# Kernel optimization log

Measured on AMD Instinct MI355X. Metric: run time of the kernel, lower is better.

The kernel has to match this reference:

```python
import jax, jax.numpy as jnp
import numpy as np

N_NODES = 102400
N_EDGES = 1638400
DIMS = [128, 64, 32, 1]  # decoder_dim=128, decoder_l=3, last layer -> 1


def setup_inputs() -> dict:
    key = jax.random.key(0)
    ks = jax.random.split(key, 10)
    inp = {
        'b_z': jax.random.normal(ks[0], (N_NODES, DIMS[0]), jnp.float32),
        'src': jax.random.randint(ks[1], (N_EDGES,), 0, N_NODES, jnp.int64 if jax.config.jax_enable_x64 else jnp.int32),
        'dst': jax.random.randint(ks[2], (N_EDGES,), 0, N_NODES, jnp.int64 if jax.config.jax_enable_x64 else jnp.int32),
        'edge_weight': jax.random.uniform(ks[3], (N_EDGES,), jnp.float32),
        'b_size': 100,
    }
    # GraphConv weights: W [in, out], bias [out] (DGL xavier init; randn ok for ref)
    for i in range(3):
        inp[f'W{i}'] = jax.random.normal(ks[4 + i], (DIMS[i], DIMS[i + 1]), jnp.float32) * (1.0 / np.sqrt(DIMS[i]))
        inp[f'b{i}'] = jnp.zeros((DIMS[i + 1],), jnp.float32)
    return inp


def _gcn_layer(h, src, dst, ew, W, b, activate):
    n = h.shape[0]
    ones = jnp.ones((src.shape[0],), h.dtype)
    # norm='both': symmetric degree normalization with plain (unweighted) degrees
    out_deg = jnp.clip(jax.ops.segment_sum(ones, src, num_segments=n), 1.0)
    in_deg = jnp.clip(jax.ops.segment_sum(ones, dst, num_segments=n), 1.0)
    h = h * (out_deg ** -0.5)[:, None]
    h = h @ W  # in_feats > out_feats: transform before aggregation (DGL order)
    msg = h[src] * ew[:, None]           # [E, out] edge-weighted gather
    agg = jax.ops.segment_sum(msg, dst, num_segments=n)  # scatter-add
    agg = agg * (in_deg ** -0.5)[:, None] + b
    return jnp.tanh(agg) if activate else agg


def reference(b_z, src, dst, edge_weight, b_size, W0, b0, W1, b1, W2, b2):
    h = b_z
    h = _gcn_layer(h, src, dst, edge_weight, W0, b0, True)
    h = _gcn_layer(h, src, dst, edge_weight, W1, b1, True)
    h = _gcn_layer(h, src, dst, edge_weight, W2, b2, False)
    return h.reshape(b_size, -1)
```

## Files before the change

kernel.cpp:

```cpp
#include <hip/hip_runtime.h>
#include <hip/hip_fp16.h>
#include <math.h>

#define N_NODES 102400
#define N_EDGES 1638400
#define NB 100
#define PB 256
#define EPB (N_EDGES/PB)

union H4 { int2 i2; __half h[4]; };

typedef _Float16 f16;
typedef __attribute__((ext_vector_type(8))) _Float16 f16x8;
typedef __attribute__((ext_vector_type(4))) float f32x4;

__global__ __launch_bounds__(256) void fusedA_kernel(
    const int* __restrict__ src, const int* __restrict__ dst,
    int* __restrict__ histD, int* __restrict__ histS,
    const float* __restrict__ h, const float* __restrict__ W, __half* __restrict__ out) {
    const int tid = threadIdx.x;

    if (blockIdx.x < PB) {
        __shared__ int hD[NB], hS[NB];
        if (tid < NB) { hD[tid] = 0; hS[tid] = 0; }
        __syncthreads();
        int base = blockIdx.x * EPB;
        for (int i = tid; i < EPB; i += 256) {
            atomicAdd(&hD[dst[base + i] >> 10], 1);
            atomicAdd(&hS[src[base + i] >> 10], 1);
        }
        __syncthreads();
        if (tid < NB) {
            histD[blockIdx.x * NB + tid] = hD[tid];
            histS[blockIdx.x * NB + tid] = hS[tid];
        }
        return;
    }

    const int lane = tid & 63;
    const int wid = tid >> 6;
    const int lr = lane & 15;
    const int kg = lane >> 4;
    const long bbase = (long)(blockIdx.x - PB) * 256 + wid * 16;

    f16x8 bf[4][4];
    #pragma unroll
    for (int ks = 0; ks < 4; ++ks)
        #pragma unroll
        for (int ct = 0; ct < 4; ++ct)
            #pragma unroll
            for (int j = 0; j < 8; ++j)
                bf[ks][ct][j] = (f16)W[(ks * 32 + kg * 8 + j) * 64 + ct * 16 + lr];

    #pragma unroll
    for (int t = 0; t < 4; ++t) {
        const long rowbase = bbase + t * 64;
        const float* hrow = h + (rowbase + lr) * 128 + kg * 8;
        f32x4 acc[4] = {{0,0,0,0},{0,0,0,0},{0,0,0,0},{0,0,0,0}};
        #pragma unroll
        for (int ks = 0; ks < 4; ++ks) {
            const float4 a0 = *(const float4*)(hrow + ks * 32);
            const float4 a1 = *(const float4*)(hrow + ks * 32 + 4);
            f16x8 af;
            af[0] = (f16)a0.x; af[1] = (f16)a0.y; af[2] = (f16)a0.z; af[3] = (f16)a0.w;
            af[4] = (f16)a1.x; af[5] = (f16)a1.y; af[6] = (f16)a1.z; af[7] = (f16)a1.w;
            #pragma unroll
            for (int ct = 0; ct < 4; ++ct)
                acc[ct] = __builtin_amdgcn_mfma_f32_16x16x32_f16(af, bf[ks][ct], acc[ct], 0, 0, 0);
        }
        #pragma unroll
        for (int ct = 0; ct < 4; ++ct)
            #pragma unroll
            for (int r = 0; r < 4; ++r)
                out[(rowbase + kg * 4 + r) * 64 + ct * 16 + lr] = __float2half_rn(acc[ct][r]);
    }
}

__global__ __launch_bounds__(256) void scanB_kernel(const int* __restrict__ histD, const int* __restrict__ histS,
                                                    int* __restrict__ offD, int* __restrict__ offS,
                                                    int* __restrict__ coarseD, int* __restrict__ coarseS) {
    __shared__ int totD[NB], totS[NB], baseD[NB + 1], baseS[NB + 1];
    int t = threadIdx.x;
    if (t < NB) { int s = 0; for (int k = 0; k < PB; k++) s += histD[k * NB + t]; totD[t] = s; }
    else if (t >= 128 && t < 128 + NB) { int j = t - 128; int s = 0; for (int k = 0; k < PB; k++) s += histS[k * NB + j]; totS[j] = s; }
    __syncthreads();
    if (t == 0)   { int r = 0; for (int j = 0; j < NB; j++) { baseD[j] = r; r += totD[j]; } baseD[NB] = r; }
    if (t == 128) { int r = 0; for (int j = 0; j < NB; j++) { baseS[j] = r; r += totS[j]; } baseS[NB] = r; }
    __syncthreads();
    if (t < NB) { int r = baseD[t]; for (int k = 0; k < PB; k++) { offD[k * NB + t] = r; r += histD[k * NB + t]; } }
    else if (t >= 128 && t < 128 + NB) { int j = t - 128; int r = baseS[j]; for (int k = 0; k < PB; k++) { offS[k * NB + j] = r; r += histS[k * NB + j]; } }
    if (t <= NB) coarseD[t] = baseD[t];
    if (t >= 128 && t <= 128 + NB) coarseS[t - 128] = baseS[t - 128];
}

__global__ __launch_bounds__(256) void partC_kernel(const int* __restrict__ src, const int* __restrict__ dst,
                                                    const float* __restrict__ ew,
                                                    const int* __restrict__ offD, const int* __restrict__ offS,
                                                    int2* __restrict__ partD, unsigned short* __restrict__ partS) {
    __shared__ int cD[NB], cS[NB];
    int tid = threadIdx.x;
    if (tid < NB) { cD[tid] = offD[blockIdx.x * NB + tid]; cS[tid] = offS[blockIdx.x * NB + tid]; }
    __syncthreads();
    int base = blockIdx.x * EPB;
    for (int i = tid; i < EPB; i += 256) {
        int s = src[base + i], d = dst[base + i];
        float w = ew[base + i];
        int p = atomicAdd(&cD[d >> 10], 1);
        partD[p] = make_int2(s | ((d & 1023) << 17), __float_as_int(w));
        int q = atomicAdd(&cS[s >> 10], 1);
        partS[q] = (unsigned short)(s & 1023);
    }
}

__global__ __launch_bounds__(1024) void fineS_kernel(const unsigned short* __restrict__ partS, const int* __restrict__ coarseS,
                                                     float* __restrict__ outdeg_inv) {
    __shared__ int hist[1024];
    int tid = threadIdx.x;
    hist[tid] = 0;
    __syncthreads();
    int beg = coarseS[blockIdx.x], end = coarseS[blockIdx.x + 1];
    for (int i = beg + tid; i < end; i += 1024) atomicAdd(&hist[partS[i]], 1);
    __syncthreads();
    outdeg_inv[blockIdx.x * 1024 + tid] = 1.0f / sqrtf((float)max(hist[tid], 1));
}

__global__ __launch_bounds__(1024) void fineD_kernel(const int2* __restrict__ partD, const int* __restrict__ coarseD,
                                                     const float* __restrict__ outdeg_inv,
                                                     int2* __restrict__ edge_perm, int* __restrict__ row_off,
                                                     float* __restrict__ indeg_inv) {
    __shared__ int hist[1024], cursor[1024];
    __shared__ int wsum[16];
    int tid = threadIdx.x, lane = tid & 63, wid = tid >> 6;
    hist[tid] = 0;
    __syncthreads();
    int beg = coarseD[blockIdx.x], end = coarseD[blockIdx.x + 1];
    for (int i = beg + tid; i < end; i += 1024) atomicAdd(&hist[(partD[i].x >> 17) & 1023], 1);
    __syncthreads();
    int v = hist[tid];
    int x = v;
    #pragma unroll
    for (int s = 1; s < 64; s <<= 1) { int t = __shfl_up(x, s, 64); if (lane >= s) x += t; }
    if (lane == 63) wsum[wid] = x;
    __syncthreads();
    if (wid == 0) {
        int ws = (lane < 16) ? wsum[lane] : 0;
        int y = ws;
        #pragma unroll
        for (int s = 1; s < 16; s <<= 1) { int t = __shfl_up(y, s, 64); if (lane >= s) y += t; }
        if (lane < 16) wsum[lane] = y - ws;
    }
    __syncthreads();
    int ex = wsum[wid] + x - v;
    cursor[tid] = beg + ex;
    int node = blockIdx.x * 1024 + tid;
    row_off[node] = beg + ex;
    indeg_inv[node] = 1.0f / sqrtf((float)max(v, 1));
    if (blockIdx.x == NB - 1 && tid == 0) row_off[N_NODES] = N_EDGES;
    __syncthreads();
    for (int i = beg + tid; i < end; i += 1024) {
        int2 t2 = partD[i];
        int d = (t2.x >> 17) & 1023, s = t2.x & 0x1FFFF;
        int p = atomicAdd(&cursor[d], 1);
        float w = __int_as_float(t2.y) * outdeg_inv[s];
        edge_perm[p] = make_int2(s, __float_as_int(w));
    }
}

__global__ __launch_bounds__(256) void agg64_gemm_kernel(
    const __half* __restrict__ ht, const int* __restrict__ row_off,
    const int2* __restrict__ ep, const float* __restrict__ indeg_inv,
    const float* __restrict__ b0, const float* __restrict__ W1,
    __half* __restrict__ ht1, int N) {
    __shared__ float h1s[8][64];
    const int tid = threadIdx.x;
    const int lane = tid & 63;
    const int wv = tid >> 6;
    const int chunk = lane & 15;
    const int eslot = lane >> 4;
    const int hf = lane >> 5;
    const int c = lane & 31;

    float w1reg[32];
    #pragma unroll
    for (int j = 0; j < 32; ++j) w1reg[j] = W1[(hf * 32 + j) * 32 + c];
    const float bch = b0[(chunk << 2) | eslot];
    const char* htb = (const char*)ht;
    const unsigned coff = (unsigned)(chunk << 3);

    const int pair0 = (blockIdx.x * blockDim.x + tid) >> 6;
    const int npairs = N >> 1;
    const int nwaves = (gridDim.x * blockDim.x) >> 6;

    for (int pid = pair0; pid < npairs; pid += nwaves) {
        const int n0 = pid << 1;
        const int ro0 = row_off[n0], ro1 = row_off[n0 + 1], ro2 = row_off[n0 + 2];
        const int em0 = max(ro1 - 1, 0), em1 = max(ro2 - 1, 0);
        float4 a0 = {0, 0, 0, 0}, a1 = {0, 0, 0, 0};
        float4 c0 = {0, 0, 0, 0}, c1 = {0, 0, 0, 0};
        int e0 = ro0, e1 = ro1;
        while (true) {
            const int i00 = e0 + eslot, i01 = i00 + 4, i02 = i00 + 8, i03 = i00 + 12;
            const int j00 = e1 + eslot, j01 = j00 + 4, j02 = j00 + 8, j03 = j00 + 12;
            int2 p00 = ep[min(i00, em0)];
            int2 p01 = ep[min(i01, em0)];
            int2 p02 = ep[min(i02, em0)];
            int2 p03 = ep[min(i03, em0)];
            int2 p10 = ep[min(j00, em1)];
            int2 p11 = ep[min(j01, em1)];
            int2 p12 = ep[min(j02, em1)];
            int2 p13 = ep[min(j03, em1)];
            float w00 = (i00 < ro1) ? __int_as_float(p00.y) : 0.0f;
            float w01 = (i01 < ro1) ? __int_as_float(p01.y) : 0.0f;
            float w02 = (i02 < ro1) ? __int_as_float(p02.y) : 0.0f;
            float w03 = (i03 < ro1) ? __int_as_float(p03.y) : 0.0f;
            float w10 = (j00 < ro2) ? __int_as_float(p10.y) : 0.0f;
            float w11 = (j01 < ro2) ? __int_as_float(p11.y) : 0.0f;
            float w12 = (j02 < ro2) ? __int_as_float(p12.y) : 0.0f;
            float w13 = (j03 < ro2) ? __int_as_float(p13.y) : 0.0f;
            H4 r00, r01, r02, r03, r10, r11, r12, r13;
            r00.i2 = *(const int2*)(htb + (((unsigned)p00.x << 7) | coff));
            r01.i2 = *(const int2*)(htb + (((unsigned)p01.x << 7) | coff));
            r02.i2 = *(const int2*)(htb + (((unsigned)p02.x << 7) | coff));
            r03.i2 = *(const int2*)(htb + (((unsigned)p03.x << 7) | coff));
            r10.i2 = *(const int2*)(htb + (((unsigned)p10.x << 7) | coff));
            r11.i2 = *(const int2*)(htb + (((unsigned)p11.x << 7) | coff));
            r12.i2 = *(const int2*)(htb + (((unsigned)p12.x << 7) | coff));
            r13.i2 = *(const int2*)(htb + (((unsigned)p13.x << 7) | coff));
            a0.x = fmaf(__half2float(r00.h[0]), w00, a0.x);
            a0.y = fmaf(__half2float(r00.h[1]), w00, a0.y);
            a0.z = fmaf(__half2float(r00.h[2]), w00, a0.z);
            a0.w = fmaf(__half2float(r00.h[3]), w00, a0.w);
            a1.x = fmaf(__half2float(r01.h[0]), w01, a1.x);
            a1.y = fmaf(__half2float(r01.h[1]), w01, a1.y);
            a1.z = fmaf(__half2float(r01.h[2]), w01, a1.z);
            a1.w = fmaf(__half2float(r01.h[3]), w01, a1.w);
            a0.x = fmaf(__half2float(r02.h[0]), w02, a0.x);
            a0.y = fmaf(__half2float(r02.h[1]), w02, a0.y);
            a0.z = fmaf(__half2float(r02.h[2]), w02, a0.z);
            a0.w = fmaf(__half2float(r02.h[3]), w02, a0.w);
            a1.x = fmaf(__half2float(r03.h[0]), w03, a1.x);
            a1.y = fmaf(__half2float(r03.h[1]), w03, a1.y);
            a1.z = fmaf(__half2float(r03.h[2]), w03, a1.z);
            a1.w = fmaf(__half2float(r03.h[3]), w03, a1.w);
            c0.x = fmaf(__half2float(r10.h[0]), w10, c0.x);
            c0.y = fmaf(__half2float(r10.h[1]), w10, c0.y);
            c0.z = fmaf(__half2float(r10.h[2]), w10, c0.z);
            c0.w = fmaf(__half2float(r10.h[3]), w10, c0.w);
            c1.x = fmaf(__half2float(r11.h[0]), w11, c1.x);
            c1.y = fmaf(__half2float(r11.h[1]), w11, c1.y);
            c1.z = fmaf(__half2float(r11.h[2]), w11, c1.z);
            c1.w = fmaf(__half2float(r11.h[3]), w11, c1.w);
            c0.x = fmaf(__half2float(r12.h[0]), w12, c0.x);
            c0.y = fmaf(__half2float(r12.h[1]), w12, c0.y);
            c0.z = fmaf(__half2float(r12.h[2]), w12, c0.z);
            c0.w = fmaf(__half2float(r12.h[3]), w12, c0.w);
            c1.x = fmaf(__half2float(r13.h[0]), w13, c1.x);
            c1.y = fmaf(__half2float(r13.h[1]), w13, c1.y);
            c1.z = fmaf(__half2float(r13.h[2]), w13, c1.z);
            c1.w = fmaf(__half2float(r13.h[3]), w13, c1.w);
            e0 += 16; e1 += 16;
            if (e0 >= ro1 && e1 >= ro2) break;
        }
        a0.x += a1.x; a0.y += a1.y; a0.z += a1.z; a0.w += a1.w;
        c0.x += c1.x; c0.y += c1.y; c0.z += c1.z; c0.w += c1.w;
        #pragma unroll
        for (int s = 16; s <= 32; s <<= 1) {
            a0.x += __shfl_xor(a0.x, s, 64);
            a0.y += __shfl_xor(a0.y, s, 64);
            a0.z += __shfl_xor(a0.z, s, 64);
            a0.w += __shfl_xor(a0.w, s, 64);
            c0.x += __shfl_xor(c0.x, s, 64);
            c0.y += __shfl_xor(c0.y, s, 64);
            c0.z += __shfl_xor(c0.z, s, 64);
            c0.w += __shfl_xor(c0.w, s, 64);
        }
        const float sc0 = indeg_inv[n0], sc1 = indeg_inv[n0 + 1];
        float v0 = (eslot == 0) ? a0.x : (eslot == 1) ? a0.y : (eslot == 2) ? a0.z : a0.w;
        float v1 = (eslot == 0) ? c0.x : (eslot == 1) ? c0.y : (eslot == 2) ? c0.z : c0.w;
        v0 = tanhf(fmaf(v0, sc0, bch));
        v1 = tanhf(fmaf(v1, sc1, bch));
        const int sl = wv << 1;
        h1s[sl][(chunk << 2) | eslot] = v0;
        h1s[sl + 1][(chunk << 2) | eslot] = v1;
        asm volatile("s_waitcnt lgkmcnt(0)" ::: "memory");
        float t0 = 0.0f, t1 = 0.0f;
        #pragma unroll
        for (int j4 = 0; j4 < 8; ++j4) {
            const float4 h0 = *(const float4*)&h1s[sl][hf * 32 + j4 * 4];
            const float4 h1 = *(const float4*)&h1s[sl + 1][hf * 32 + j4 * 4];
            t0 = fmaf(h0.x, w1reg[j4 * 4 + 0], t0);
            t0 = fmaf(h0.y, w1reg[j4 * 4 + 1], t0);
            t0 = fmaf(h0.z, w1reg[j4 * 4 + 2], t0);
            t0 = fmaf(h0.w, w1reg[j4 * 4 + 3], t0);
            t1 = fmaf(h1.x, w1reg[j4 * 4 + 0], t1);
            t1 = fmaf(h1.y, w1reg[j4 * 4 + 1], t1);
            t1 = fmaf(h1.z, w1reg[j4 * 4 + 2], t1);
            t1 = fmaf(h1.w, w1reg[j4 * 4 + 3], t1);
        }
        t0 += __shfl_xor(t0, 32, 64);
        t1 += __shfl_xor(t1, 32, 64);
        if (hf == 0) {
            ht1[(long)n0 * 32 + c] = __float2half_rn(t0);
            ht1[(long)(n0 + 1) * 32 + c] = __float2half_rn(t1);
        }
    }
}

__global__ __launch_bounds__(256) void agg32_dot_kernel(const __half* __restrict__ ht, const int* __restrict__ row_off,
                                 const int2* __restrict__ ep,
                                 const float* __restrict__ indeg_inv, const float* __restrict__ bias,
                                 const float* __restrict__ W2, float* __restrict__ ht2, int N) {
    int quad = (blockIdx.x * blockDim.x + threadIdx.x) >> 6;
    int lane = threadIdx.x & 63;
    int n0 = quad << 2;
    if (n0 >= N) return;
    int chunk = lane & 7;
    int eslot = lane >> 3;
    int ro0 = row_off[n0], ro1 = row_off[n0 + 1], ro2 = row_off[n0 + 2];
    int ro3 = row_off[n0 + 3], ro4 = row_off[n0 + 4];
    int em0 = max(ro1 - 1, 0), em1 = max(ro2 - 1, 0);
    int em2 = max(ro3 - 1, 0), em3 = max(ro4 - 1, 0);
    const char* htb = (const char*)ht;
    unsigned coff = (unsigned)(chunk << 3);
    float4 a0 = {0, 0, 0, 0}, a1 = {0, 0, 0, 0};
    float4 b0 = {0, 0, 0, 0}, b1 = {0, 0, 0, 0};
    float4 c0 = {0, 0, 0, 0}, c1 = {0, 0, 0, 0};
    float4 d0 = {0, 0, 0, 0}, d1 = {0, 0, 0, 0};
    int e0 = ro0, e1 = ro1, e2 = ro2, e3 = ro3;
    while (e0 < ro1 || e1 < ro2 || e2 < ro3 || e3 < ro4) {
        int i00 = e0 + eslot, i01 = i00 + 8;
        int i10 = e1 + eslot, i11 = i10 + 8;
        int i20 = e2 + eslot, i21 = i20 + 8;
        int i30 = e3 + eslot, i31 = i30 + 8;
        int2 p00 = ep[min(i00, em0)];
        int2 p01 = ep[min(i01, em0)];
        int2 p10 = ep[min(i10, em1)];
        int2 p11 = ep[min(i11, em1)];
        int2 p20 = ep[min(i20, em2)];
        int2 p21 = ep[min(i21, em2)];
        int2 p30 = ep[min(i30, em3)];
        int2 p31 = ep[min(i31, em3)];
        float w00 = (i00 < ro1) ? __int_as_float(p00.y) : 0.0f;
        float w01 = (i01 < ro1) ? __int_as_float(p01.y) : 0.0f;
        float w10 = (i10 < ro2) ? __int_as_float(p10.y) : 0.0f;
        float w11 = (i11 < ro2) ? __int_as_float(p11.y) : 0.0f;
        float w20 = (i20 < ro3) ? __int_as_float(p20.y) : 0.0f;
        float w21 = (i21 < ro3) ? __int_as_float(p21.y) : 0.0f;
        float w30 = (i30 < ro4) ? __int_as_float(p30.y) : 0.0f;
        float w31 = (i31 < ro4) ? __int_as_float(p31.y) : 0.0f;
        H4 r00, r01, r10, r11, r20, r21, r30, r31;
        r00.i2 = *(const int2*)(htb + (((unsigned)p00.x << 6) | coff));
        r01.i2 = *(const int2*)(htb + (((unsigned)p01.x << 6) | coff));
        r10.i2 = *(const int2*)(htb + (((unsigned)p10.x << 6) | coff));
        r11.i2 = *(const int2*)(htb + (((unsigned)p11.x << 6) | coff));
        r20.i2 = *(const int2*)(htb + (((unsigned)p20.x << 6) | coff));
        r21.i2 = *(const int2*)(htb + (((unsigned)p21.x << 6) | coff));
        r30.i2 = *(const int2*)(htb + (((unsigned)p30.x << 6) | coff));
        r31.i2 = *(const int2*)(htb + (((unsigned)p31.x << 6) | coff));
        a0.x = fmaf(__half2float(r00.h[0]), w00, a0.x);
        a0.y = fmaf(__half2float(r00.h[1]), w00, a0.y);
        a0.z = fmaf(__half2float(r00.h[2]), w00, a0.z);
        a0.w = fmaf(__half2float(r00.h[3]), w00, a0.w);
        a1.x = fmaf(__half2float(r01.h[0]), w01, a1.x);
        a1.y = fmaf(__half2float(r01.h[1]), w01, a1.y);
        a1.z = fmaf(__half2float(r01.h[2]), w01, a1.z);
        a1.w = fmaf(__half2float(r01.h[3]), w01, a1.w);
        b0.x = fmaf(__half2float(r10.h[0]), w10, b0.x);
        b0.y = fmaf(__half2float(r10.h[1]), w10, b0.y);
        b0.z = fmaf(__half2float(r10.h[2]), w10, b0.z);
        b0.w = fmaf(__half2float(r10.h[3]), w10, b0.w);
        b1.x = fmaf(__half2float(r11.h[0]), w11, b1.x);
        b1.y = fmaf(__half2float(r11.h[1]), w11, b1.y);
        b1.z = fmaf(__half2float(r11.h[2]), w11, b1.z);
        b1.w = fmaf(__half2float(r11.h[3]), w11, b1.w);
        c0.x = fmaf(__half2float(r20.h[0]), w20, c0.x);
        c0.y = fmaf(__half2float(r20.h[1]), w20, c0.y);
        c0.z = fmaf(__half2float(r20.h[2]), w20, c0.z);
        c0.w = fmaf(__half2float(r20.h[3]), w20, c0.w);
        c1.x = fmaf(__half2float(r21.h[0]), w21, c1.x);
        c1.y = fmaf(__half2float(r21.h[1]), w21, c1.y);
        c1.z = fmaf(__half2float(r21.h[2]), w21, c1.z);
        c1.w = fmaf(__half2float(r21.h[3]), w21, c1.w);
        d0.x = fmaf(__half2float(r30.h[0]), w30, d0.x);
        d0.y = fmaf(__half2float(r30.h[1]), w30, d0.y);
        d0.z = fmaf(__half2float(r30.h[2]), w30, d0.z);
        d0.w = fmaf(__half2float(r30.h[3]), w30, d0.w);
        d1.x = fmaf(__half2float(r31.h[0]), w31, d1.x);
        d1.y = fmaf(__half2float(r31.h[1]), w31, d1.y);
        d1.z = fmaf(__half2float(r31.h[2]), w31, d1.z);
        d1.w = fmaf(__half2float(r31.h[3]), w31, d1.w);
        e0 += 16; e1 += 16; e2 += 16; e3 += 16;
    }
    a0.x += a1.x; a0.y += a1.y; a0.z += a1.z; a0.w += a1.w;
    b0.x += b1.x; b0.y += b1.y; b0.z += b1.z; b0.w += b1.w;
    c0.x += c1.x; c0.y += c1.y; c0.z += c1.z; c0.w += c1.w;
    d0.x += d1.x; d0.y += d1.y; d0.z += d1.z; d0.w += d1.w;
    #pragma unroll
    for (int s = 8; s <= 32; s <<= 1) {
        a0.x += __shfl_xor(a0.x, s, 64);
        a0.y += __shfl_xor(a0.y, s, 64);
        a0.z += __shfl_xor(a0.z, s, 64);
        a0.w += __shfl_xor(a0.w, s, 64);
        b0.x += __shfl_xor(b0.x, s, 64);
        b0.y += __shfl_xor(b0.y, s, 64);
        b0.z += __shfl_xor(b0.z, s, 64);
        b0.w += __shfl_xor(b0.w, s, 64);
        c0.x += __shfl_xor(c0.x, s, 64);
        c0.y += __shfl_xor(c0.y, s, 64);
        c0.z += __shfl_xor(c0.z, s, 64);
        c0.w += __shfl_xor(c0.w, s, 64);
        d0.x += __shfl_xor(d0.x, s, 64);
        d0.y += __shfl_xor(d0.y, s, 64);
        d0.z += __shfl_xor(d0.z, s, 64);
        d0.w += __shfl_xor(d0.w, s, 64);
    }
    int q = eslot & 3;
    int ch = (chunk << 2) | q;
    float bb = bias[ch], ww = W2[ch];
    float s0 = indeg_inv[n0], s1 = indeg_inv[n0 + 1], s2 = indeg_inv[n0 + 2], s3 = indeg_inv[n0 + 3];
    float v0 = (q == 0) ? a0.x : (q == 1) ? a0.y : (q == 2) ? a0.z : a0.w;
    float v1 = (q == 0) ? b0.x : (q == 1) ? b0.y : (q == 2) ? b0.z : b0.w;
    float v2 = (q == 0) ? c0.x : (q == 1) ? c0.y : (q == 2) ? c0.z : c0.w;
    float v3 = (q == 0) ? d0.x : (q == 1) ? d0.y : (q == 2) ? d0.z : d0.w;
    float t0 = tanhf(fmaf(v0, s0, bb)) * ww;
    float t1 = tanhf(fmaf(v1, s1, bb)) * ww;
    float t2 = tanhf(fmaf(v2, s2, bb)) * ww;
    float t3 = tanhf(fmaf(v3, s3, bb)) * ww;
    #pragma unroll
    for (int s = 1; s <= 32; s <<= 1) {
        t0 += __shfl_xor(t0, s, 64);
        t1 += __shfl_xor(t1, s, 64);
        t2 += __shfl_xor(t2, s, 64);
        t3 += __shfl_xor(t3, s, 64);
    }
    if (lane == 0) {
        ht2[n0] = 0.5f * t0;
        ht2[n0 + 1] = 0.5f * t1;
        ht2[n0 + 2] = 0.5f * t2;
        ht2[n0 + 3] = 0.5f * t3;
    }
}

__global__ void agg1_kernel(const float* __restrict__ ht2, const int* __restrict__ row_off,
                            const int2* __restrict__ ep,
                            const float* __restrict__ indeg_inv, const float* __restrict__ bias,
                            float* __restrict__ out, int N) {
    int wave = (blockIdx.x * blockDim.x + threadIdx.x) >> 6;
    int lane = threadIdx.x & 63;
    int sub = lane >> 4;
    int slot = lane & 15;
    int node = wave * 4 + sub;
    if (node >= N) return;
    int beg = row_off[node], end = row_off[node + 1];
    float acc = 0.0f;
    for (int e = beg + slot; e < end; e += 16) {
        int2 t = ep[e];
        acc += ht2[t.x] * __int_as_float(t.y);
    }
    #pragma unroll
    for (int s = 1; s <= 8; s <<= 1) acc += __shfl_xor(acc, s, 64);
    if (slot == 0) out[node] = acc * indeg_inv[node] + bias[0];
}

extern "C" void kernel_launch(void* const* d_in, const int* in_sizes, int n_in,
                              void* d_out, int out_size, void* d_ws, size_t ws_size,
                              hipStream_t stream) {
    const float* b_z = (const float*)d_in[0];
    const int*   src = (const int*)d_in[1];
    const int*   dst = (const int*)d_in[2];
    const float* ew  = (const float*)d_in[3];
    const float* W0 = (const float*)d_in[5];
    const float* b0 = (const float*)d_in[6];
    const float* W1 = (const float*)d_in[7];
    const float* b1 = (const float*)d_in[8];
    const float* W2 = (const float*)d_in[9];
    const float* b2 = (const float*)d_in[10];
    float* out = (float*)d_out;

    const int N = N_NODES;
    const int E = N_EDGES;

    char* p = (char*)d_ws;
    int*   row_off    = (int*)p;            p += (size_t)(N + 4) * 4;
    float* outdeg_inv = (float*)p;          p += (size_t)N * 4;
    float* indeg_inv  = (float*)p;          p += (size_t)N * 4;
    int*   histD      = (int*)p;            p += (size_t)PB * NB * 4;
    int*   histS      = (int*)p;            p += (size_t)PB * NB * 4;
    int*   offD       = (int*)p;            p += (size_t)PB * NB * 4;
    int*   offS       = (int*)p;            p += (size_t)PB * NB * 4;
    int*   coarseD    = (int*)p;            p += (size_t)(NB + 4) * 4;
    int*   coarseS    = (int*)p;            p += (size_t)(NB + 4) * 4;
    int2*  edge_perm  = (int2*)p;           p += (size_t)E * 8;
    char*  bufP       = p;                  p += (size_t)E * 8;
    char*  bufS       = p;                  p += (size_t)E * 2;
    char*  bufH       = p;
    int2*           partD = (int2*)bufP;
    __half*         ht1   = (__half*)bufP;
    unsigned short* partS = (unsigned short*)bufS;
    float*          ht2   = (float*)bufS;
    __half*         ht    = (__half*)bufH;

    fusedA_kernel<<<PB + N / 256, 256, 0, stream>>>(src, dst, histD, histS, b_z, W0, ht);

    scanB_kernel<<<1, 256, 0, stream>>>(histD, histS, offD, offS, coarseD, coarseS);
    partC_kernel<<<PB, 256, 0, stream>>>(src, dst, ew, offD, offS, partD, partS);
    fineS_kernel<<<NB, 1024, 0, stream>>>(partS, coarseS, outdeg_inv);
    fineD_kernel<<<NB, 1024, 0, stream>>>(partD, coarseD, outdeg_inv, edge_perm, row_off, indeg_inv);

    agg64_gemm_kernel<<<4096, 256, 0, stream>>>(ht, row_off, edge_perm, indeg_inv, b0, W1, ht1, N);

    agg32_dot_kernel<<<N / 16, 256, 0, stream>>>(ht1, row_off, edge_perm, indeg_inv, b1, W2, ht2, N);

    agg1_kernel<<<N / 16, 256, 0, stream>>>(ht2, row_off, edge_perm, indeg_inv, b2, out, N);
}
```

Measured before the change: 321.8 us.

## Double coarse bucket count, transpose histogram layout, vectorize scan and partition

Raises the coarse bucket count from 100 to 200, so buckets cover 512 nodes and the fine kernels run 200 blocks of 512 threads. This spreads the work over more CUs. The per-block histograms are stored bucket-major, so the single-block scan reads and writes contiguous int4 rows instead of strided columns. The partition kernel also loads src, dst and weights as int4/float4. The risk is more shared-memory atomics per bucket and larger histogram arrays.

After: 345.9 us. 1.07x slower.

```diff
diff --git a/kernel.cpp b/kernel.cpp
--- a/kernel.cpp
+++ b/kernel.cpp
@@ -4,7 +4,7 @@
 
 #define N_NODES 102400
 #define N_EDGES 1638400
-#define NB 100
+#define NB 200
 #define PB 256
 #define EPB (N_EDGES/PB)
 
@@ -26,13 +26,13 @@
         __syncthreads();
         int base = blockIdx.x * EPB;
         for (int i = tid; i < EPB; i += 256) {
-            atomicAdd(&hD[dst[base + i] >> 10], 1);
-            atomicAdd(&hS[src[base + i] >> 10], 1);
+            atomicAdd(&hD[dst[base + i] >> 9], 1);
+            atomicAdd(&hS[src[base + i] >> 9], 1);
         }
         __syncthreads();
         if (tid < NB) {
-            histD[blockIdx.x * NB + tid] = hD[tid];
-            histS[blockIdx.x * NB + tid] = hS[tid];
+            histD[tid * PB + blockIdx.x] = hD[tid];
+            histS[tid * PB + blockIdx.x] = hS[tid];
         }
         return;
     }
@@ -81,16 +81,42 @@
                                                     int* __restrict__ coarseD, int* __restrict__ coarseS) {
     __shared__ int totD[NB], totS[NB], baseD[NB + 1], baseS[NB + 1];
     int t = threadIdx.x;
-    if (t < NB) { int s = 0; for (int k = 0; k < PB; k++) s += histD[k * NB + t]; totD[t] = s; }
-    else if (t >= 128 && t < 128 + NB) { int j = t - 128; int s = 0; for (int k = 0; k < PB; k++) s += histS[k * NB + j]; totS[j] = s; }
+    for (int j = t; j < NB; j += 256) {
+        const int4* rd = (const int4*)(histD + j * PB);
+        const int4* rs = (const int4*)(histS + j * PB);
+        int sd = 0, ss = 0;
+        #pragma unroll 8
+        for (int k = 0; k < PB / 4; ++k) {
+            int4 a = rd[k]; sd += a.x + a.y + a.z + a.w;
+            int4 b = rs[k]; ss += b.x + b.y + b.z + b.w;
+        }
+        totD[j] = sd; totS[j] = ss;
+    }
     __syncthreads();
     if (t == 0)   { int r = 0; for (int j = 0; j < NB; j++) { baseD[j] = r; r += totD[j]; } baseD[NB] = r; }
     if (t == 128) { int r = 0; for (int j = 0; j < NB; j++) { baseS[j] = r; r += totS[j]; } baseS[NB] = r; }
     __syncthreads();
-    if (t < NB) { int r = baseD[t]; for (int k = 0; k < PB; k++) { offD[k * NB + t] = r; r += histD[k * NB + t]; } }
-    else if (t >= 128 && t < 128 + NB) { int j = t - 128; int r = baseS[j]; for (int k = 0; k < PB; k++) { offS[k * NB + j] = r; r += histS[k * NB + j]; } }
-    if (t <= NB) coarseD[t] = baseD[t];
-    if (t >= 128 && t <= 128 + NB) coarseS[t - 128] = baseS[t - 128];
+    for (int j = t; j < NB; j += 256) {
+        int r = baseD[j];
+        const int4* rd = (const int4*)(histD + j * PB);
+        int4* od = (int4*)(offD + j * PB);
+        #pragma unroll 8
+        for (int k = 0; k < PB / 4; ++k) {
+            int4 a = rd[k]; int4 o;
+            o.x = r; r += a.x; o.y = r; r += a.y; o.z = r; r += a.z; o.w = r; r += a.w;
+            od[k] = o;
+        }
+        int r2 = baseS[j];
+        const int4* rs = (const int4*)(histS + j * PB);
+        int4* os = (int4*)(offS + j * PB);
+        #pragma unroll 8
+        for (int k = 0; k < PB / 4; ++k) {
+            int4 a = rs[k]; int4 o;
+            o.x = r2; r2 += a.x; o.y = r2; r2 += a.y; o.z = r2; r2 += a.z; o.w = r2; r2 += a.w;
+            os[k] = o;
+        }
+    }
+    if (t <= NB) { coarseD[t] = baseD[t]; coarseS[t] = baseS[t]; }
 }
 
 __global__ __launch_bounds__(256) void partC_kernel(const int* __restrict__ src, const int* __restrict__ dst,
@@ -99,42 +125,56 @@
                                                     int2* __restrict__ partD, unsigned short* __restrict__ partS) {
     __shared__ int cD[NB], cS[NB];
     int tid = threadIdx.x;
-    if (tid < NB) { cD[tid] = offD[blockIdx.x * NB + tid]; cS[tid] = offS[blockIdx.x * NB + tid]; }
+    if (tid < NB) { cD[tid] = offD[tid * PB + blockIdx.x]; cS[tid] = offS[tid * PB + blockIdx.x]; }
     __syncthreads();
     int base = blockIdx.x * EPB;
-    for (int i = tid; i < EPB; i += 256) {
-        int s = src[base + i], d = dst[base + i];
-        float w = ew[base + i];
-        int p = atomicAdd(&cD[d >> 10], 1);
-        partD[p] = make_int2(s | ((d & 1023) << 17), __float_as_int(w));
-        int q = atomicAdd(&cS[s >> 10], 1);
-        partS[q] = (unsigned short)(s & 1023);
-    }
-}
-
-__global__ __launch_bounds__(1024) void fineS_kernel(const unsigned short* __restrict__ partS, const int* __restrict__ coarseS,
-                                                     float* __restrict__ outdeg_inv) {
-    __shared__ int hist[1024];
+    for (int i4 = tid; i4 < EPB / 4; i4 += 256) {
+        int4 s4 = *(const int4*)(src + base + i4 * 4);
+        int4 d4 = *(const int4*)(dst + base + i4 * 4);
+        float4 w4 = *(const float4*)(ew + base + i4 * 4);
+        int p, q;
+        p = atomicAdd(&cD[d4.x >> 9], 1);
+        partD[p] = make_int2(s4.x | ((d4.x & 511) << 17), __float_as_int(w4.x));
+        q = atomicAdd(&cS[s4.x >> 9], 1);
+        partS[q] = (unsigned short)(s4.x & 511);
+        p = atomicAdd(&cD[d4.y >> 9], 1);
+        partD[p] = make_int2(s4.y | ((d4.y & 511) << 17), __float_as_int(w4.y));
+        q = atomicAdd(&cS[s4.y >> 9], 1);
+        partS[q] = (unsigned short)(s4.y & 511);
+        p = atomicAdd(&cD[d4.z >> 9], 1);
+        partD[p] = make_int2(s4.z | ((d4.z & 511) << 17), __float_as_int(w4.z));
+        q = atomicAdd(&cS[s4.z >> 9], 1);
+        partS[q] = (unsigned short)(s4.z & 511);
+        p = atomicAdd(&cD[d4.w >> 9], 1);
+        partD[p] = make_int2(s4.w | ((d4.w & 511) << 17), __float_as_int(w4.w));
+        q = atomicAdd(&cS[s4.w >> 9], 1);
+        partS[q] = (unsigned short)(s4.w & 511);
+    }
+}
+
+__global__ __launch_bounds__(512) void fineS_kernel(const unsigned short* __restrict__ partS, const int* __restrict__ coarseS,
+                                                    float* __restrict__ outdeg_inv) {
+    __shared__ int hist[512];
     int tid = threadIdx.x;
     hist[tid] = 0;
     __syncthreads();
     int beg = coarseS[blockIdx.x], end = coarseS[blockIdx.x + 1];
-    for (int i = beg + tid; i < end; i += 1024) atomicAdd(&hist[partS[i]], 1);
-    __syncthreads();
-    outdeg_inv[blockIdx.x * 1024 + tid] = 1.0f / sqrtf((float)max(hist[tid], 1));
-}
-
-__global__ __launch_bounds__(1024) void fineD_kernel(const int2* __restrict__ partD, const int* __restrict__ coarseD,
-                                                     const float* __restrict__ outdeg_inv,
-                                                     int2* __restrict__ edge_perm, int* __restrict__ row_off,
-                                                     float* __restrict__ indeg_inv) {
-    __shared__ int hist[1024], cursor[1024];
-    __shared__ int wsum[16];
+    for (int i = beg + tid; i < end; i += 512) atomicAdd(&hist[partS[i]], 1);
+    __syncthreads();
+    outdeg_inv[blockIdx.x * 512 + tid] = 1.0f / sqrtf((float)max(hist[tid], 1));
+}
+
+__global__ __launch_bounds__(512) void fineD_kernel(const int2* __restrict__ partD, const int* __restrict__ coarseD,
+                                                    const float* __restrict__ outdeg_inv,
+                                                    int2* __restrict__ edge_perm, int* __restrict__ row_off,
+                                                    float* __restrict__ indeg_inv) {
+    __shared__ int hist[512], cursor[512];
+    __shared__ int wsum[8];
     int tid = threadIdx.x, lane = tid & 63, wid = tid >> 6;
     hist[tid] = 0;
     __syncthreads();
     int beg = coarseD[blockIdx.x], end = coarseD[blockIdx.x + 1];
-    for (int i = beg + tid; i < end; i += 1024) atomicAdd(&hist[(partD[i].x >> 17) & 1023], 1);
+    for (int i = beg + tid; i < end; i += 512) atomicAdd(&hist[(partD[i].x >> 17) & 511], 1);
     __syncthreads();
     int v = hist[tid];
     int x = v;
@@ -143,23 +183,23 @@
     if (lane == 63) wsum[wid] = x;
     __syncthreads();
     if (wid == 0) {
-        int ws = (lane < 16) ? wsum[lane] : 0;
+        int ws = (lane < 8) ? wsum[lane] : 0;
         int y = ws;
         #pragma unroll
-        for (int s = 1; s < 16; s <<= 1) { int t = __shfl_up(y, s, 64); if (lane >= s) y += t; }
-        if (lane < 16) wsum[lane] = y - ws;
+        for (int s = 1; s < 8; s <<= 1) { int t = __shfl_up(y, s, 64); if (lane >= s) y += t; }
+        if (lane < 8) wsum[lane] = y - ws;
     }
     __syncthreads();
     int ex = wsum[wid] + x - v;
     cursor[tid] = beg + ex;
-    int node = blockIdx.x * 1024 + tid;
+    int node = blockIdx.x * 512 + tid;
     row_off[node] = beg + ex;
     indeg_inv[node] = 1.0f / sqrtf((float)max(v, 1));
     if (blockIdx.x == NB - 1 && tid == 0) row_off[N_NODES] = N_EDGES;
     __syncthreads();
-    for (int i = beg + tid; i < end; i += 1024) {
+    for (int i = beg + tid; i < end; i += 512) {
         int2 t2 = partD[i];
-        int d = (t2.x >> 17) & 1023, s = t2.x & 0x1FFFF;
+        int d = (t2.x >> 17) & 511, s = t2.x & 0x1FFFF;
         int p = atomicAdd(&cursor[d], 1);
         float w = __int_as_float(t2.y) * outdeg_inv[s];
         edge_perm[p] = make_int2(s, __float_as_int(w));
@@ -484,12 +524,12 @@
     int*   row_off    = (int*)p;            p += (size_t)(N + 4) * 4;
     float* outdeg_inv = (float*)p;          p += (size_t)N * 4;
     float* indeg_inv  = (float*)p;          p += (size_t)N * 4;
-    int*   histD      = (int*)p;            p += (size_t)PB * NB * 4;
-    int*   histS      = (int*)p;            p += (size_t)PB * NB * 4;
-    int*   offD       = (int*)p;            p += (size_t)PB * NB * 4;
-    int*   offS       = (int*)p;            p += (size_t)PB * NB * 4;
-    int*   coarseD    = (int*)p;            p += (size_t)(NB + 4) * 4;
-    int*   coarseS    = (int*)p;            p += (size_t)(NB + 4) * 4;
+    int*   histD      = (int*)p;            p += (size_t)NB * PB * 4;
+    int*   histS      = (int*)p;            p += (size_t)NB * PB * 4;
+    int*   offD       = (int*)p;            p += (size_t)NB * PB * 4;
+    int*   offS       = (int*)p;            p += (size_t)NB * PB * 4;
+    int*   coarseD    = (int*)p;            p += (size_t)(NB + 8) * 4;
+    int*   coarseS    = (int*)p;            p += (size_t)(NB + 8) * 4;
     int2*  edge_perm  = (int2*)p;           p += (size_t)E * 8;
     char*  bufP       = p;                  p += (size_t)E * 8;
     char*  bufS       = p;                  p += (size_t)E * 2;
@@ -504,8 +544,8 @@
 
     scanB_kernel<<<1, 256, 0, stream>>>(histD, histS, offD, offS, coarseD, coarseS);
     partC_kernel<<<PB, 256, 0, stream>>>(src, dst, ew, offD, offS, partD, partS);
-    fineS_kernel<<<NB, 1024, 0, stream>>>(partS, coarseS, outdeg_inv);
-    fineD_kernel<<<NB, 1024, 0, stream>>>(partD, coarseD, outdeg_inv, edge_perm, row_off, indeg_inv);
+    fineS_kernel<<<NB, 512, 0, stream>>>(partS, coarseS, outdeg_inv);
+    fineD_kernel<<<NB, 512, 0, stream>>>(partD, coarseD, outdeg_inv, edge_perm, row_off, indeg_inv);
 
     agg64_gemm_kernel<<<4096, 256, 0, stream>>>(ht, row_off, edge_perm, indeg_inv, b0, W1, ht1, N);
 
```
